# Kernel tuning notes

Measured on AMD Instinct MI355X. Metric: run time of the kernel, lower is better.

The kernel has to match this reference:

```python
import jax, jax.numpy as jnp
import numpy as np

IN_FEATURES = 4096
OUT_FEATURES = 11008
N_TOKENS = 32


def setup_inputs() -> dict:
    key = jax.random.key(0)
    k_x, k_w, k_s, k_b = jax.random.split(key, 4)
    x = jax.random.normal(k_x, (N_TOKENS, IN_FEATURES), dtype=jnp.float16)
    # int8 quantized weight, [out_features, in_features]
    qweight = jax.random.randint(k_w, (OUT_FEATURES, IN_FEATURES), -128, 128, dtype=jnp.int8)
    # per-output-channel scales, small positive fp16
    scales = (jax.random.uniform(k_s, (OUT_FEATURES,), dtype=jnp.float32) * 0.01 + 1e-4).astype(jnp.float16)
    bias = (jax.random.normal(k_b, (OUT_FEATURES,), dtype=jnp.float32) * 0.01).astype(jnp.float16)
    return {"x": x, "qweight": qweight, "scales": scales, "bias": bias}


def reference(x, qweight, scales, bias):
    # Dequantize: fp16 weight = int8 * per-row scale  -> [out, in]
    w = (qweight.astype(jnp.float16) * scales[:, None]).astype(jnp.float16)
    # out[t, o] = sum_i x[t, i] * w[o, i]
    out = jnp.einsum("ti,oi->to", x, w) + bias[None, :]
    return out.astype(jnp.float16)
```

## Files before the change

kernel.cpp:

```cpp
#include <hip/hip_runtime.h>
#include <hip/hip_bf16.h>


constexpr int IN_F   = 4096;
constexpr int OUT_F  = 11008;
constexpr int KSLICE = 512;
constexpr int CK     = 128;

typedef short bf16x8 __attribute__((ext_vector_type(8)));
typedef float f32x4  __attribute__((ext_vector_type(4)));

union B8 { bf16x8 v; unsigned u[4]; };

__device__ __forceinline__ unsigned pack2f(float lo, float hi) {
    return __builtin_amdgcn_perm(__float_as_uint(hi),
                                 __float_as_uint(lo),
                                 0x07060302u);
}

__global__ __launch_bounds__(256)
void xconv_kernel(const float* __restrict__ x, unsigned* __restrict__ xb) {
    const int i = (blockIdx.x * 256 + threadIdx.x) * 4;
    float4 v = *reinterpret_cast<const float4*>(x + i);
    xb[i / 2]     = pack2f(v.x, v.y);
    xb[i / 2 + 1] = pack2f(v.z, v.w);
}

__global__ __launch_bounds__(512, 4)
void qlin_kernel(const unsigned short* __restrict__ xb,
                 const int* __restrict__ w,
                 const float* __restrict__ scales,
                 const float* __restrict__ bias,
                 float* __restrict__ out)
{
    __shared__ int   wbuf[8][CK * 16];
    __shared__ float red[7][2][4][64];

    const int lane = threadIdx.x & 63;
    const int wv   = threadIdx.x >> 6;
    const int r    = lane & 15;
    const int q    = lane >> 4;

    const int n0 = blockIdx.x << 4;
    const int kb = wv * KSLICE;

    f32x4 acc0 = {0.f, 0.f, 0.f, 0.f};
    f32x4 acc1 = {0.f, 0.f, 0.f, 0.f};

    const unsigned short* xp0 = xb + r * IN_F + kb + q * 8;
    const unsigned short* xp1 = xp0 + 16 * IN_F;

    const int  swz = r & 7;
    const int4* lsp = reinterpret_cast<const int4*>(&wbuf[wv][0]) + r * 32;

    for (int c = 0; c < KSLICE / CK; ++c) {
        const int kc = kb + c * CK;
        #pragma unroll
        for (int j = 0; j < 8; ++j) {
            const int rj = 2 * j + (lane >> 5);
            const int gj = (lane & 31) ^ (rj & 7);
            const int* src = w + (size_t)(n0 + rj) * IN_F + kc + 4 * gj;
            __builtin_amdgcn_global_load_lds(
                (const __attribute__((address_space(1))) void*)src,
                (__attribute__((address_space(3))) void*)&wbuf[wv][j * 256],
                16, 0, 0);
        }
        bf16x8 af0[4], af1[4];
        #pragma unroll
        for (int i = 0; i < 4; ++i) {
            af0[i] = *reinterpret_cast<const bf16x8*>(xp0 + c * CK + i * 32);
            af1[i] = *reinterpret_cast<const bf16x8*>(xp1 + c * CK + i * 32);
        }
        __syncthreads();

        #pragma unroll
        for (int i = 0; i < 4; ++i) {
            const int G0 = i * 8 + q * 2;
            int4 qa = lsp[G0 ^ swz];
            int4 qb = lsp[(G0 + 1) ^ swz];
            B8 bb;
            bb.u[0] = pack2f((float)qa.x, (float)qa.y);
            bb.u[1] = pack2f((float)qa.z, (float)qa.w);
            bb.u[2] = pack2f((float)qb.x, (float)qb.y);
            bb.u[3] = pack2f((float)qb.z, (float)qb.w);
            acc0 = __builtin_amdgcn_mfma_f32_16x16x32_bf16(af0[i], bb.v, acc0, 0, 0, 0);
            acc1 = __builtin_amdgcn_mfma_f32_16x16x32_bf16(af1[i], bb.v, acc1, 0, 0, 0);
        }
        __syncthreads();
    }

    if (wv > 0) {
        #pragma unroll
        for (int i = 0; i < 4; ++i) {
            red[wv - 1][0][i][lane] = acc0[i];
            red[wv - 1][1][i][lane] = acc1[i];
        }
    }
    __syncthreads();
    if (wv == 0) {
        #pragma unroll
        for (int j = 0; j < 7; ++j) {
            #pragma unroll
            for (int i = 0; i < 4; ++i) {
                acc0[i] += red[j][0][i][lane];
                acc1[i] += red[j][1][i][lane];
            }
        }
        const int n = n0 + r;
        const float s = scales[n];
        const float b = bias[n];
        #pragma unroll
        for (int i = 0; i < 4; ++i) {
            out[(q * 4 + i) * OUT_F + n]      = acc0[i] * s + b;
            out[(16 + q * 4 + i) * OUT_F + n] = acc1[i] * s + b;
        }
    }
}

extern "C" void kernel_launch(void* const* d_in, const int* in_sizes, int n_in,
                              void* d_out, int out_size, void* d_ws, size_t ws_size,
                              hipStream_t stream) {
    const float* x      = (const float*)d_in[0];
    const int*   w      = (const int*)d_in[1];
    const float* scales = (const float*)d_in[2];
    const float* bias   = (const float*)d_in[3];
    float*       out    = (float*)d_out;
    unsigned*    xb     = (unsigned*)d_ws;

    xconv_kernel<<<dim3(32 * IN_F / (256 * 4)), dim3(256), 0, stream>>>(x, xb);
    qlin_kernel<<<dim3(OUT_F / 16), dim3(512), 0, stream>>>(
        (const unsigned short*)xb, w, scales, bias, out);
}
```

Measured before the change: 252.3 us.

## Fuse activation bf16 conversion into GEMV kernel and halve waves per block

Removes the separate x-to-bf16 conversion kernel and converts fp32 activations to bf16 inline inside the main kernel. Each block now uses 4 waves with a 1024-wide K slice instead of 8 waves with 512, shrinking LDS and the cross-wave reduction. The per-chunk __syncthreads are replaced with a vmcnt wait plus sched barrier, since each wave only reads its own LDS slice. The trade-off is redundant activation conversion work in every block, twice the fp32 activation bytes loaded per block, and fewer waves to hide memory latency.

```diff
diff --git a/kernel.cpp b/kernel.cpp
--- a/kernel.cpp
+++ b/kernel.cpp
@@ -1,11 +1,11 @@
 #include <hip/hip_runtime.h>
-#include <hip/hip_bf16.h>
 
 
 constexpr int IN_F   = 4096;
 constexpr int OUT_F  = 11008;
-constexpr int KSLICE = 512;
+constexpr int KSLICE = 1024;
 constexpr int CK     = 128;
+constexpr int NCHUNK = KSLICE / CK;
 
 typedef short bf16x8 __attribute__((ext_vector_type(8)));
 typedef float f32x4  __attribute__((ext_vector_type(4)));
@@ -18,23 +18,15 @@
                                  0x07060302u);
 }
 
-__global__ __launch_bounds__(256)
-void xconv_kernel(const float* __restrict__ x, unsigned* __restrict__ xb) {
-    const int i = (blockIdx.x * 256 + threadIdx.x) * 4;
-    float4 v = *reinterpret_cast<const float4*>(x + i);
-    xb[i / 2]     = pack2f(v.x, v.y);
-    xb[i / 2 + 1] = pack2f(v.z, v.w);
-}
-
-__global__ __launch_bounds__(512, 4)
-void qlin_kernel(const unsigned short* __restrict__ xb,
+__global__ __launch_bounds__(256, 4)
+void qlin_kernel(const float* __restrict__ x,
                  const int* __restrict__ w,
                  const float* __restrict__ scales,
                  const float* __restrict__ bias,
                  float* __restrict__ out)
 {
-    __shared__ int   wbuf[8][CK * 16];
-    __shared__ float red[7][2][4][64];
+    __shared__ int   wbuf[4][CK * 16];
+    __shared__ float red[3][2][4][64];
 
     const int lane = threadIdx.x & 63;
     const int wv   = threadIdx.x >> 6;
@@ -47,13 +39,13 @@
     f32x4 acc0 = {0.f, 0.f, 0.f, 0.f};
     f32x4 acc1 = {0.f, 0.f, 0.f, 0.f};
 
-    const unsigned short* xp0 = xb + r * IN_F + kb + q * 8;
-    const unsigned short* xp1 = xp0 + 16 * IN_F;
+    const float* xp0 = x + r * IN_F + kb + q * 8;
+    const float* xp1 = xp0 + 16 * IN_F;
 
     const int  swz = r & 7;
     const int4* lsp = reinterpret_cast<const int4*>(&wbuf[wv][0]) + r * 32;
 
-    for (int c = 0; c < KSLICE / CK; ++c) {
+    for (int c = 0; c < NCHUNK; ++c) {
         const int kc = kb + c * CK;
         #pragma unroll
         for (int j = 0; j < 8; ++j) {
@@ -68,10 +60,20 @@
         bf16x8 af0[4], af1[4];
         #pragma unroll
         for (int i = 0; i < 4; ++i) {
-            af0[i] = *reinterpret_cast<const bf16x8*>(xp0 + c * CK + i * 32);
-            af1[i] = *reinterpret_cast<const bf16x8*>(xp1 + c * CK + i * 32);
+            const float4* pa = reinterpret_cast<const float4*>(xp0 + c * CK + i * 32);
+            const float4* pb = reinterpret_cast<const float4*>(xp1 + c * CK + i * 32);
+            const float4 a0 = pa[0], a1 = pa[1];
+            const float4 b0 = pb[0], b1 = pb[1];
+            B8 fa, fb;
+            fa.u[0] = pack2f(a0.x, a0.y); fa.u[1] = pack2f(a0.z, a0.w);
+            fa.u[2] = pack2f(a1.x, a1.y); fa.u[3] = pack2f(a1.z, a1.w);
+            fb.u[0] = pack2f(b0.x, b0.y); fb.u[1] = pack2f(b0.z, b0.w);
+            fb.u[2] = pack2f(b1.x, b1.y); fb.u[3] = pack2f(b1.z, b1.w);
+            af0[i] = fa.v;
+            af1[i] = fb.v;
         }
-        __syncthreads();
+        asm volatile("s_waitcnt vmcnt(0)" ::: "memory");
+        __builtin_amdgcn_sched_barrier(0);
 
         #pragma unroll
         for (int i = 0; i < 4; ++i) {
@@ -86,7 +88,6 @@
             acc0 = __builtin_amdgcn_mfma_f32_16x16x32_bf16(af0[i], bb.v, acc0, 0, 0, 0);
             acc1 = __builtin_amdgcn_mfma_f32_16x16x32_bf16(af1[i], bb.v, acc1, 0, 0, 0);
         }
-        __syncthreads();
     }
 
     if (wv > 0) {
@@ -99,7 +100,7 @@
     __syncthreads();
     if (wv == 0) {
         #pragma unroll
-        for (int j = 0; j < 7; ++j) {
+        for (int j = 0; j < 3; ++j) {
             #pragma unroll
             for (int i = 0; i < 4; ++i) {
                 acc0[i] += red[j][0][i][lane];
@@ -125,9 +126,8 @@
     const float* scales = (const float*)d_in[2];
     const float* bias   = (const float*)d_in[3];
     float*       out    = (float*)d_out;
-    unsigned*    xb     = (unsigned*)d_ws;
+    (void)d_ws; (void)ws_size;
 
-    xconv_kernel<<<dim3(32 * IN_F / (256 * 4)), dim3(256), 0, stream>>>(x, xb);
-    qlin_kernel<<<dim3(OUT_F / 16), dim3(512), 0, stream>>>(
-        (const unsigned short*)xb, w, scales, bias, out);
+    qlin_kernel<<<dim3(OUT_F / 16), dim3(256), 0, stream>>>(
+        x, w, scales, bias, out);
 }
```

After: 265.8 us. +5.3%, slower.
